# Optimization experiments

Measured on AMD Instinct MI355X. Metric: run time of the kernel, lower is better.

## Reference

```python
import jax, jax.numpy as jnp
import numpy as np

B, N, K, C, H, W = 2, 8, 8, 256, 96, 96
CTX = C + K + 4 * K + 13  # 309
HID = 256
ALPHA = 0.3          # REFINE_EMA_ALPHA
TEMP = 1.0           # READOUT_TEMPERATURE
SIM_HIGH, SIM_LOW = 0.8, 0.3
A_KEEP, A_REFINE, A_REPLACE, A_SPAWN = 0, 1, 2, 3


def _l2norm(x, axis=-1, eps=1e-12):
    return x / jnp.maximum(jnp.linalg.norm(x, axis=axis, keepdims=True), eps)


def setup_inputs() -> dict:
    key = jax.random.key(0)
    ks = jax.random.split(key, 12)
    value = jax.random.normal(ks[0], (B, N, C, H, W), jnp.float32)
    frame_feat = jax.random.normal(ks[1], (B, C, H, W), jnp.float32)
    mask = jax.random.uniform(ks[2], (B, N, H, W), jnp.float32)
    proto = jax.random.normal(ks[3], (B, N, K, C), jnp.float32)
    age = jax.random.uniform(ks[4], (B, N, K), jnp.float32) * 10.0
    usage = jax.random.uniform(ks[5], (B, N, K), jnp.float32) * 5.0
    conf = jax.random.uniform(ks[6], (B, N, K), jnp.float32)
    valid = jax.random.randint(ks[7], (B, N, K), 0, 2).astype(bool)
    W1 = jax.random.normal(ks[8], (CTX, HID), jnp.float32) * 0.02
    b1 = jnp.zeros((HID,), jnp.float32)
    W2 = jax.random.normal(ks[9], (HID, 4), jnp.float32) * 0.02
    b2 = jnp.zeros((4,), jnp.float32)
    proto_gate = jnp.float32(1.0)
    frame_gate = jnp.float32(1.0)
    return dict(value=value, frame_feat=frame_feat, mask=mask, proto=proto,
                age=age, usage=usage, conf=conf, W1=W1, b1=b1, W2=W2, b2=b2,
                proto_gate=proto_gate, frame_gate=frame_gate, valid=valid)


def reference(value, frame_feat, mask, proto, age, usage, conf,
              W1, b1, W2, b2, proto_gate, frame_gate, valid):
    # ---- candidate prototype via masked pooling (PROTO_POOLING='mask') ----
    fv = value.reshape(B, N, C, H * W)                      # [B,N,C,HW]
    fm = mask.reshape(B, N, 1, H * W)                       # [B,N,1,HW]
    denom = jnp.maximum(fm.sum(-1), 1e-6)                   # [B,N,1]
    cand = (fv * fm).sum(-1) / denom                        # [B,N,C]
    mask_strength = fm.mean(-1)[..., 0]                     # [B,N]
    fallback = fv.mean(-1)
    cand = jnp.where((denom[..., 0] <= 1e-5)[..., None], fallback, cand)
    cand = _l2norm(cand)

    # ---- uncertainty features (prev_mask is None -> temporal term = 0) ----
    m = jnp.clip(mask, 1e-4, 1.0 - 1e-4)
    ent = -(m * jnp.log(m) + (1.0 - m) * jnp.log(1.0 - m))
    fg_prob = m.mean((-2, -1))
    fg_area = (m > 0.5).astype(jnp.float32).mean((-2, -1))
    gx = jnp.abs(m[..., 1:, :] - m[..., :-1, :]).mean((-2, -1))
    gy = jnp.abs(m[..., :, 1:] - m[..., :, :-1]).mean((-2, -1))
    unc = jnp.stack([ent.mean((-2, -1)), fg_prob, fg_area,
                     0.5 * (gx + gy), jnp.zeros_like(fg_prob)], -1)  # [B,N,5]

    # ---- context / similarity ----
    bank_n = _l2norm(proto)                                  # [B,N,K,C]
    sim = jnp.einsum('bnc,bnkc->bnk', cand, bank_n)
    sim = jnp.where(valid, sim, -1.0)
    g_t = jnp.broadcast_to(frame_feat.mean((2, 3))[:, None, :], (B, N, C))
    age_n = age / jnp.maximum(age.max(), 1.0)
    usage_n = usage / jnp.maximum(usage.max(), 1.0)
    bank_stats = jnp.stack([valid.astype(jnp.float32), age_n, usage_n, conf], -1)
    top2 = jax.lax.top_k(sim, 2)[0]
    t1, t2 = top2[..., 0], top2[..., 1]
    glob = jnp.stack([valid.astype(jnp.float32).mean(-1), age_n.max(-1),
                      usage_n.min(-1), conf.mean(-1), conf.max(-1)], -1)
    context = jnp.concatenate([g_t, sim, bank_stats.reshape(B, N, 4 * K),
                               jnp.stack([t1, t2, t1 - t2], -1), glob, unc], -1)
    logits = jax.nn.gelu(context @ W1 + b1, approximate=False) @ W2 + b2  # [B,N,4]

    any_valid = valid.any(-1)
    target_slot = jnp.where(any_valid, sim.argmax(-1), 0)
    max_sim = jnp.take_along_axis(sim, target_slot[..., None], -1)[..., 0]
    max_sim = jnp.where(any_valid, max_sim, -1.0)

    # ---- rule-based action selection ----
    action = jnp.where(~any_valid, A_SPAWN,
             jnp.where(max_sim >= SIM_HIGH, A_REFINE,
             jnp.where(max_sim >= SIM_LOW, A_KEEP, A_SPAWN)))

    # ---- victim / slot selection ----
    victim = (age_n + (1.0 - usage_n) + (1.0 - conf)).argmax(-1)
    first_empty = (~valid).argmax(-1)
    spawn_slot = jnp.where((~valid).any(-1), first_empty, victim)
    upd_slot = jnp.where(action == A_REFINE, target_slot, spawn_slot)

    # ---- policy-gated EMA scatter update of the bank ----
    onehot = jax.nn.one_hot(upd_slot, K, dtype=bool)                 # [B,N,K]
    refine_m = onehot & (action == A_REFINE)[..., None]
    write_m = onehot & (action == A_SPAWN)[..., None]
    refined = _l2norm((1.0 - ALPHA) * proto + ALPHA * cand[:, :, None, :])
    cand_b = jnp.broadcast_to(cand[:, :, None, :], proto.shape)
    proto_new = jnp.where(refine_m[..., None], refined,
                jnp.where(write_m[..., None], cand_b, proto))
    upd_m = refine_m | write_m
    age_new = jnp.where(upd_m, 0.0, age + 1.0)
    usage_new = usage + upd_m.astype(jnp.float32)
    conf_new = jnp.where(write_m, mask_strength[..., None],
               jnp.where(refine_m, jnp.maximum(conf, max_sim[..., None]), conf))
    valid_new = valid | write_m

    # ---- prototype-conditioned readout ----
    bank_nn = _l2norm(proto_new)                                      # [B,N,K,C]
    vn = value / jnp.maximum(jnp.linalg.norm(value, axis=2, keepdims=True), 1e-12)
    rsim = jnp.einsum('bnkc,bnchw->bnkhw', bank_nn, vn)
    rlog = jnp.where(valid_new[..., None, None], rsim / TEMP, -1e9)
    attn = jax.nn.softmax(rlog, axis=2)
    attn = attn * valid_new.any(-1)[..., None, None, None].astype(jnp.float32)
    proto_map = jnp.einsum('bnkhw,bnkc->bnchw', attn, proto_new)
    conditioned = value + proto_gate * proto_map + frame_gate * frame_feat[:, None]
    return conditioned
```

## Files before the change

### kernel.cpp

```cpp
#include <hip/hip_runtime.h>
#include <math.h>

constexpr int Bc = 2, Nc = 8, Kc = 8, Cc = 256, HWc = 96 * 96;
constexpr int BN = Bc * Nc;
constexpr int HW2 = HWc / 2;
constexpr float ALPHA = 0.3f;
constexpr float SIM_HIGH = 0.8f, SIM_LOW = 0.3f;

__device__ __forceinline__ float wred_sum_all(float v) {
#pragma unroll
  for (int o = 32; o > 0; o >>= 1) v += __shfl_xor(v, o, 64);
  return v;
}
__device__ __forceinline__ float wred_sum(float v) {
#pragma unroll
  for (int o = 32; o > 0; o >>= 1) v += __shfl_down(v, o, 64);
  return v;
}
__device__ __forceinline__ float wred_max(float v) {
#pragma unroll
  for (int o = 32; o > 0; o >>= 1) v = fmaxf(v, __shfl_down(v, o, 64));
  return v;
}
__device__ __forceinline__ float bred_sum(float v, float* sc) {
  int lane = threadIdx.x & 63, wid = threadIdx.x >> 6;
  v = wred_sum(v);
  __syncthreads();
  if (lane == 0) sc[wid] = v;
  __syncthreads();
  return sc[0] + sc[1] + sc[2] + sc[3];
}
__device__ __forceinline__ float bred_max(float v, float* sc) {
  int lane = threadIdx.x & 63, wid = threadIdx.x >> 6;
  v = wred_max(v);
  __syncthreads();
  if (lane == 0) sc[wid] = v;
  __syncthreads();
  return fmaxf(fmaxf(sc[0], sc[1]), fmaxf(sc[2], sc[3]));
}

__global__ __launch_bounds__(256) void k1_sums(const float* __restrict__ value,
                                               const float* __restrict__ mask,
                                               float* __restrict__ sum_v,
                                               float* __restrict__ sum_vm) {
  const int bnc = blockIdx.x;
  const int bn = bnc >> 8;
  const int tid = threadIdx.x;
  const float4* v4 = (const float4*)(value + (size_t)bnc * HWc);
  const float4* m4 = (const float4*)(mask + (size_t)bn * HWc);
  float av = 0.f, avm = 0.f;
#pragma unroll
  for (int i = 0; i < 9; ++i) {
    float4 v = v4[i * 256 + tid];
    float4 m = m4[i * 256 + tid];
    av += v.x + v.y + v.z + v.w;
    avm += v.x * m.x + v.y * m.y + v.z * m.z + v.w * m.w;
  }
  __shared__ float sc[8];
  float rv = wred_sum(av);
  float rvm = wred_sum(avm);
  int lane = tid & 63, wid = tid >> 6;
  if (lane == 0) { sc[wid] = rv; sc[4 + wid] = rvm; }
  __syncthreads();
  if (tid == 0) {
    sum_v[bnc] = sc[0] + sc[1] + sc[2] + sc[3];
    sum_vm[bnc] = sc[4] + sc[5] + sc[6] + sc[7];
  }
}

__global__ __launch_bounds__(256) void k2_update(
    const float* __restrict__ mask, const float* __restrict__ proto,
    const float* __restrict__ age, const float* __restrict__ usage,
    const float* __restrict__ conf, const int* __restrict__ valid,
    const float* __restrict__ sum_v, const float* __restrict__ sum_vm,
    float* __restrict__ proto_new, float* __restrict__ bank_nn,
    float* __restrict__ validf) {
  const int bn = blockIdx.x;
  const int tid = threadIdx.x;
  const int lane = tid & 63, w = tid >> 6;
  __shared__ float sc[4];
  __shared__ float s_cand[Cc];
  __shared__ float s_sim[Kc];
  __shared__ int s_slot, s_ref, s_wr;

  float a = (tid < BN * Kc) ? age[tid] : -3e38f;
  float u = (tid < BN * Kc) ? usage[tid] : -3e38f;
  const float age_den = fmaxf(bred_max(a, sc), 1.0f);
  const float usage_den = fmaxf(bred_max(u, sc), 1.0f);

  float ms = 0.f;
  const float* mrow = mask + (size_t)bn * HWc;
  for (int i = tid; i < HWc; i += 256) ms += mrow[i];
  const float msum = bred_sum(ms, sc);
  const float denom = fmaxf(msum, 1e-6f);

  const int c = tid;
  const float sv = sum_v[bn * Cc + c];
  const float svm = sum_vm[bn * Cc + c];
  float cand = (denom <= 1e-5f) ? (sv * (1.0f / HWc)) : (svm / denom);
  const float css = bred_sum(cand * cand, sc);
  s_cand[c] = cand / fmaxf(sqrtf(css), 1e-12f);
  __syncthreads();

  const float4* cand4 = (const float4*)s_cand;
  const float4 c4 = cand4[lane];

#pragma unroll
  for (int kk = 0; kk < 2; ++kk) {
    const int k = w + kk * 4;
    const float4 p4 = ((const float4*)(proto + ((size_t)bn * Kc + k) * Cc))[lane];
    const float pss = wred_sum_all(p4.x * p4.x + p4.y * p4.y + p4.z * p4.z + p4.w * p4.w);
    const float pd  = wred_sum_all(p4.x * c4.x + p4.y * c4.y + p4.z * c4.z + p4.w * c4.w);
    if (lane == 0)
      s_sim[k] = (valid[bn * Kc + k] != 0) ? (pd / fmaxf(sqrtf(pss), 1e-12f)) : -1.0f;
  }
  __syncthreads();

  if (tid == 0) {
    bool anyv = false;
    for (int k = 0; k < Kc; ++k) anyv = anyv || (valid[bn * Kc + k] != 0);
    int tslot = 0; float best = s_sim[0];
    for (int k = 1; k < Kc; ++k)
      if (s_sim[k] > best) { best = s_sim[k]; tslot = k; }
    const float max_sim = anyv ? best : -1.0f;
    const int action = (!anyv) ? 3 : (max_sim >= SIM_HIGH ? 1 : (max_sim >= SIM_LOW ? 0 : 3));
    int victim = 0; float vb = -3e38f;
    for (int k = 0; k < Kc; ++k) {
      const float s = age[bn * Kc + k] / age_den + (1.f - usage[bn * Kc + k] / usage_den) +
                      (1.f - conf[bn * Kc + k]);
      if (s > vb) { vb = s; victim = k; }
    }
    int fe = 0; bool hasE = false;
    for (int k = 0; k < Kc; ++k)
      if (valid[bn * Kc + k] == 0) { fe = k; hasE = true; break; }
    const int spawn = hasE ? fe : victim;
    s_slot = (action == 1) ? tslot : spawn;
    s_ref = (action == 1);
    s_wr = (action == 3);
  }
  __syncthreads();

#pragma unroll
  for (int kk = 0; kk < 2; ++kk) {
    const int k = w + kk * 4;
    const float4 p4 = ((const float4*)(proto + ((size_t)bn * Kc + k) * Cc))[lane];
    float4 pn;
    if (k == s_slot && s_ref) {
      float4 t;
      t.x = (1.0f - ALPHA) * p4.x + ALPHA * c4.x;
      t.y = (1.0f - ALPHA) * p4.y + ALPHA * c4.y;
      t.z = (1.0f - ALPHA) * p4.z + ALPHA * c4.z;
      t.w = (1.0f - ALPHA) * p4.w + ALPHA * c4.w;
      const float tss = wred_sum_all(t.x * t.x + t.y * t.y + t.z * t.z + t.w * t.w);
      const float inv = 1.0f / fmaxf(sqrtf(tss), 1e-12f);
      pn.x = t.x * inv; pn.y = t.y * inv; pn.z = t.z * inv; pn.w = t.w * inv;
    } else if (k == s_slot && s_wr) {
      pn = c4;
    } else {
      pn = p4;
    }
    ((float4*)(proto_new + ((size_t)bn * Kc + k) * Cc))[lane] = pn;
    const float bss = wred_sum_all(pn.x * pn.x + pn.y * pn.y + pn.z * pn.z + pn.w * pn.w);
    const float binv = 1.0f / fmaxf(sqrtf(bss), 1e-12f);
    float4 bnv;
    bnv.x = pn.x * binv; bnv.y = pn.y * binv; bnv.z = pn.z * binv; bnv.w = pn.w * binv;
    ((float4*)(bank_nn + ((size_t)bn * Kc + k) * Cc))[lane] = bnv;
  }
  if (tid < Kc) {
    const int k = tid;
    const int vn = (valid[bn * Kc + k] != 0) || (s_wr && k == s_slot);
    validf[bn * Kc + k] = vn ? 1.0f : 0.0f;
  }
}

__global__ __launch_bounds__(256) void k3_readout(
    const float* __restrict__ value, const float* __restrict__ frame,
    const float* __restrict__ proto_new, const float* __restrict__ bank_nn,
    const float* __restrict__ validf, const float* __restrict__ pgp,
    const float* __restrict__ fgp, float* __restrict__ out) {
  const int bn = blockIdx.x / 72;
  const int tile = blockIdx.x % 72;
  const int b = bn >> 3;
  const int tid = threadIdx.x;
  const int lane = tid & 63, w = tid >> 6;
  const int p2 = tile * 64 + lane;

  __shared__ float s_bank[Kc * Cc];
  __shared__ float s_pn[Kc * Cc];
  __shared__ float s_part[4][9][128];
  __shared__ float s_attn[Kc][128];
  __shared__ float s_vld[Kc];

  const float* bsrc = bank_nn + (size_t)bn * Kc * Cc;
  const float* psrc = proto_new + (size_t)bn * Kc * Cc;
  for (int i = tid; i < Kc * Cc; i += 256) {
    const int k = i >> 8, c = i & 255;
    s_bank[c * 8 + k] = bsrc[i];
    s_pn[c * 8 + k] = psrc[i];
  }
  if (tid < Kc) s_vld[tid] = validf[bn * Kc + tid];
  __syncthreads();

  const float pg = pgp[0], fg = fgp[0];
  const float2* v2 = (const float2*)(value + (size_t)bn * Cc * HWc);
  const float2* f2 = (const float2*)(frame + (size_t)b * Cc * HWc);
  float2* o2 = (float2*)(out + (size_t)bn * Cc * HWc);
  const float4* bk4 = (const float4*)s_bank;
  const float4* pn4 = (const float4*)s_pn;

  float ss0 = 0.f, ss1 = 0.f;
  float d0[8], d1[8];
#pragma unroll
  for (int k = 0; k < 8; ++k) { d0[k] = 0.f; d1[k] = 0.f; }

#pragma unroll 8
  for (int c0 = 0; c0 < 64; ++c0) {
    const int c = (w << 6) + c0;
    const float2 v = v2[c * HW2 + p2];
    const float4 ba = bk4[c * 2 + 0];
    const float4 bb = bk4[c * 2 + 1];
    ss0 += v.x * v.x; ss1 += v.y * v.y;
    d0[0] += ba.x * v.x; d0[1] += ba.y * v.x; d0[2] += ba.z * v.x; d0[3] += ba.w * v.x;
    d0[4] += bb.x * v.x; d0[5] += bb.y * v.x; d0[6] += bb.z * v.x; d0[7] += bb.w * v.x;
    d1[0] += ba.x * v.y; d1[1] += ba.y * v.y; d1[2] += ba.z * v.y; d1[3] += ba.w * v.y;
    d1[4] += bb.x * v.y; d1[5] += bb.y * v.y; d1[6] += bb.z * v.y; d1[7] += bb.w * v.y;
  }
#pragma unroll
  for (int k = 0; k < 8; ++k)
    ((float2*)&s_part[w][k][0])[lane] = make_float2(d0[k], d1[k]);
  ((float2*)&s_part[w][8][0])[lane] = make_float2(ss0, ss1);
  __syncthreads();

  if (tid < 128) {
    float dd[9];
#pragma unroll
    for (int j = 0; j < 9; ++j)
      dd[j] = s_part[0][j][tid] + s_part[1][j][tid] + s_part[2][j][tid] + s_part[3][j][tid];
    const float rn = 1.0f / fmaxf(sqrtf(dd[8]), 1e-12f);
    float m = -3e38f;
#pragma unroll
    for (int k = 0; k < 8; ++k) {
      dd[k] *= rn;
      if (s_vld[k] > 0.5f) m = fmaxf(m, dd[k]);
    }
    float e[8], sum = 0.f;
#pragma unroll
    for (int k = 0; k < 8; ++k) {
      e[k] = (s_vld[k] > 0.5f) ? __expf(dd[k] - m) : 0.f;
      sum += e[k];
    }
    const float inv = (sum > 0.f) ? 1.0f / sum : 0.f;
#pragma unroll
    for (int k = 0; k < 8; ++k) s_attn[k][tid] = e[k] * inv;
  }
  __syncthreads();

  float a0[8], a1[8];
#pragma unroll
  for (int k = 0; k < 8; ++k) {
    const float2 t = ((const float2*)&s_attn[k][0])[lane];
    a0[k] = t.x; a1[k] = t.y;
  }

#pragma unroll 4
  for (int c0 = 0; c0 < 64; ++c0) {
    const int c = (w << 6) + c0;
    const float2 v = v2[c * HW2 + p2];
    const float2 f = f2[c * HW2 + p2];
    const float4 pa = pn4[c * 2 + 0];
    const float4 pb = pn4[c * 2 + 1];
    const float pm0 = a0[0] * pa.x + a0[1] * pa.y + a0[2] * pa.z + a0[3] * pa.w +
                      a0[4] * pb.x + a0[5] * pb.y + a0[6] * pb.z + a0[7] * pb.w;
    const float pm1 = a1[0] * pa.x + a1[1] * pa.y + a1[2] * pa.z + a1[3] * pa.w +
                      a1[4] * pb.x + a1[5] * pb.y + a1[6] * pb.z + a1[7] * pb.w;
    float2 o;
    o.x = v.x + pg * pm0 + fg * f.x;
    o.y = v.y + pg * pm1 + fg * f.y;
    o2[c * HW2 + p2] = o;
  }
}

extern "C" void kernel_launch(void* const* d_in, const int* in_sizes, int n_in,
                              void* d_out, int out_size, void* d_ws, size_t ws_size,
                              hipStream_t stream) {
  const float* value = (const float*)d_in[0];
  const float* frame = (const float*)d_in[1];
  const float* mask  = (const float*)d_in[2];
  const float* proto = (const float*)d_in[3];
  const float* age   = (const float*)d_in[4];
  const float* usage = (const float*)d_in[5];
  const float* conf  = (const float*)d_in[6];
  const float* pg = (const float*)d_in[11];
  const float* fg = (const float*)d_in[12];
  const int* valid = (const int*)d_in[13];
  float* out = (float*)d_out;

  float* w = (float*)d_ws;
  float* sum_v     = w;
  float* sum_vm    = w + 4096;
  float* proto_new = w + 8192;
  float* bank_nn   = w + 40960;
  float* validf    = w + 73728;

  hipLaunchKernelGGL(k1_sums, dim3(BN * Cc), dim3(256), 0, stream,
                     value, mask, sum_v, sum_vm);
  hipLaunchKernelGGL(k2_update, dim3(BN), dim3(256), 0, stream,
                     mask, proto, age, usage, conf, valid, sum_v, sum_vm,
                     proto_new, bank_nn, validf);
  hipLaunchKernelGGL(k3_readout, dim3(BN * 72), dim3(256), 0, stream,
                     value, frame, proto_new, bank_nn, validf, pg, fg, out);
}
```

Baseline: 390.2 us.

## Restructure readout kernel: channel groups within wave, shuffle reductions, fold bank normalization

```diff
diff --git a/kernel.cpp b/kernel.cpp
--- a/kernel.cpp
+++ b/kernel.cpp
@@ -6,6 +6,13 @@
 constexpr int HW2 = HWc / 2;
 constexpr float ALPHA = 0.3f;
 constexpr float SIM_HIGH = 0.8f, SIM_LOW = 0.3f;
+
+constexpr int CG = 8;
+constexpr int CPG = Cc / CG;
+constexpr int PPW = 64 / CG;
+constexpr int PPB = PPW * 4;
+constexpr int TILES = HW2 / PPB;
+constexpr int CGSTRIDE = CPG * 8 + 4;
 
 __device__ __forceinline__ float wred_sum_all(float v) {
 #pragma unroll
@@ -73,7 +80,7 @@
     const float* __restrict__ age, const float* __restrict__ usage,
     const float* __restrict__ conf, const int* __restrict__ valid,
     const float* __restrict__ sum_v, const float* __restrict__ sum_vm,
-    float* __restrict__ proto_new, float* __restrict__ bank_nn,
+    float* __restrict__ proto_new, float* __restrict__ bank_inv,
     float* __restrict__ validf) {
   const int bn = blockIdx.x;
   const int tid = threadIdx.x;
@@ -89,8 +96,11 @@
   const float usage_den = fmaxf(bred_max(u, sc), 1.0f);
 
   float ms = 0.f;
-  const float* mrow = mask + (size_t)bn * HWc;
-  for (int i = tid; i < HWc; i += 256) ms += mrow[i];
+  const float4* m4 = (const float4*)(mask + (size_t)bn * HWc);
+  for (int i = tid; i < HWc / 4; i += 256) {
+    const float4 mm = m4[i];
+    ms += (mm.x + mm.y) + (mm.z + mm.w);
+  }
   const float msum = bred_sum(ms, sc);
   const float denom = fmaxf(msum, 1e-6f);
 
@@ -161,10 +171,7 @@
     }
     ((float4*)(proto_new + ((size_t)bn * Kc + k) * Cc))[lane] = pn;
     const float bss = wred_sum_all(pn.x * pn.x + pn.y * pn.y + pn.z * pn.z + pn.w * pn.w);
-    const float binv = 1.0f / fmaxf(sqrtf(bss), 1e-12f);
-    float4 bnv;
-    bnv.x = pn.x * binv; bnv.y = pn.y * binv; bnv.z = pn.z * binv; bnv.w = pn.w * binv;
-    ((float4*)(bank_nn + ((size_t)bn * Kc + k) * Cc))[lane] = bnv;
+    if (lane == 0) bank_inv[bn * Kc + k] = 1.0f / fmaxf(sqrtf(bss), 1e-12f);
   }
   if (tid < Kc) {
     const int k = tid;
@@ -173,110 +180,107 @@
   }
 }
 
-__global__ __launch_bounds__(256) void k3_readout(
+__global__ __launch_bounds__(256, 8) void k3_readout(
     const float* __restrict__ value, const float* __restrict__ frame,
-    const float* __restrict__ proto_new, const float* __restrict__ bank_nn,
+    const float* __restrict__ proto_new, const float* __restrict__ bank_inv,
     const float* __restrict__ validf, const float* __restrict__ pgp,
     const float* __restrict__ fgp, float* __restrict__ out) {
-  const int bn = blockIdx.x / 72;
-  const int tile = blockIdx.x % 72;
+  const int bn = blockIdx.x / TILES;
+  const int tile = blockIdx.x % TILES;
   const int b = bn >> 3;
   const int tid = threadIdx.x;
   const int lane = tid & 63, w = tid >> 6;
-  const int p2 = tile * 64 + lane;
-
-  __shared__ float s_bank[Kc * Cc];
-  __shared__ float s_pn[Kc * Cc];
-  __shared__ float s_part[4][9][128];
-  __shared__ float s_attn[Kc][128];
+  const int cg = lane >> 3;
+  const int pl = lane & 7;
+  const int p2 = tile * PPB + w * PPW + pl;
+
+  __shared__ float s_pn[CG * CGSTRIDE];
+  __shared__ float s_inv[Kc];
   __shared__ float s_vld[Kc];
 
-  const float* bsrc = bank_nn + (size_t)bn * Kc * Cc;
   const float* psrc = proto_new + (size_t)bn * Kc * Cc;
   for (int i = tid; i < Kc * Cc; i += 256) {
     const int k = i >> 8, c = i & 255;
-    s_bank[c * 8 + k] = bsrc[i];
-    s_pn[c * 8 + k] = psrc[i];
-  }
-  if (tid < Kc) s_vld[tid] = validf[bn * Kc + tid];
+    s_pn[(c >> 5) * CGSTRIDE + (c & 31) * 8 + k] = psrc[i];
+  }
+  if (tid < Kc) {
+    s_inv[tid] = bank_inv[bn * Kc + tid];
+    s_vld[tid] = validf[bn * Kc + tid];
+  }
   __syncthreads();
 
   const float pg = pgp[0], fg = fgp[0];
   const float2* v2 = (const float2*)(value + (size_t)bn * Cc * HWc);
   const float2* f2 = (const float2*)(frame + (size_t)b * Cc * HWc);
   float2* o2 = (float2*)(out + (size_t)bn * Cc * HWc);
-  const float4* bk4 = (const float4*)s_bank;
-  const float4* pn4 = (const float4*)s_pn;
+  const size_t base = (size_t)(cg * CPG) * HW2 + p2;
+  const float4* pn4 = (const float4*)(s_pn + cg * CGSTRIDE);
 
   float ss0 = 0.f, ss1 = 0.f;
   float d0[8], d1[8];
 #pragma unroll
   for (int k = 0; k < 8; ++k) { d0[k] = 0.f; d1[k] = 0.f; }
 
-#pragma unroll 8
-  for (int c0 = 0; c0 < 64; ++c0) {
-    const int c = (w << 6) + c0;
-    const float2 v = v2[c * HW2 + p2];
-    const float4 ba = bk4[c * 2 + 0];
-    const float4 bb = bk4[c * 2 + 1];
+#pragma unroll 4
+  for (int i = 0; i < CPG; ++i) {
+    const float2 v = v2[base + (size_t)i * HW2];
+    const float4 ba = pn4[i * 2 + 0];
+    const float4 bb = pn4[i * 2 + 1];
     ss0 += v.x * v.x; ss1 += v.y * v.y;
     d0[0] += ba.x * v.x; d0[1] += ba.y * v.x; d0[2] += ba.z * v.x; d0[3] += ba.w * v.x;
     d0[4] += bb.x * v.x; d0[5] += bb.y * v.x; d0[6] += bb.z * v.x; d0[7] += bb.w * v.x;
     d1[0] += ba.x * v.y; d1[1] += ba.y * v.y; d1[2] += ba.z * v.y; d1[3] += ba.w * v.y;
     d1[4] += bb.x * v.y; d1[5] += bb.y * v.y; d1[6] += bb.z * v.y; d1[7] += bb.w * v.y;
   }
-#pragma unroll
-  for (int k = 0; k < 8; ++k)
-    ((float2*)&s_part[w][k][0])[lane] = make_float2(d0[k], d1[k]);
-  ((float2*)&s_part[w][8][0])[lane] = make_float2(ss0, ss1);
-  __syncthreads();
-
-  if (tid < 128) {
-    float dd[9];
-#pragma unroll
-    for (int j = 0; j < 9; ++j)
-      dd[j] = s_part[0][j][tid] + s_part[1][j][tid] + s_part[2][j][tid] + s_part[3][j][tid];
-    const float rn = 1.0f / fmaxf(sqrtf(dd[8]), 1e-12f);
-    float m = -3e38f;
-#pragma unroll
-    for (int k = 0; k < 8; ++k) {
-      dd[k] *= rn;
-      if (s_vld[k] > 0.5f) m = fmaxf(m, dd[k]);
-    }
-    float e[8], sum = 0.f;
-#pragma unroll
-    for (int k = 0; k < 8; ++k) {
-      e[k] = (s_vld[k] > 0.5f) ? __expf(dd[k] - m) : 0.f;
-      sum += e[k];
-    }
-    const float inv = (sum > 0.f) ? 1.0f / sum : 0.f;
-#pragma unroll
-    for (int k = 0; k < 8; ++k) s_attn[k][tid] = e[k] * inv;
-  }
-  __syncthreads();
-
-  float a0[8], a1[8];
+
 #pragma unroll
   for (int k = 0; k < 8; ++k) {
-    const float2 t = ((const float2*)&s_attn[k][0])[lane];
-    a0[k] = t.x; a1[k] = t.y;
-  }
+    d0[k] += __shfl_xor(d0[k], 8, 64);
+    d0[k] += __shfl_xor(d0[k], 16, 64);
+    d0[k] += __shfl_xor(d0[k], 32, 64);
+    d1[k] += __shfl_xor(d1[k], 8, 64);
+    d1[k] += __shfl_xor(d1[k], 16, 64);
+    d1[k] += __shfl_xor(d1[k], 32, 64);
+  }
+  ss0 += __shfl_xor(ss0, 8, 64); ss0 += __shfl_xor(ss0, 16, 64); ss0 += __shfl_xor(ss0, 32, 64);
+  ss1 += __shfl_xor(ss1, 8, 64); ss1 += __shfl_xor(ss1, 16, 64); ss1 += __shfl_xor(ss1, 32, 64);
+
+  const float rn0 = 1.0f / fmaxf(sqrtf(ss0), 1e-12f);
+  const float rn1 = 1.0f / fmaxf(sqrtf(ss1), 1e-12f);
+  float m0 = -3e38f, m1 = -3e38f;
+#pragma unroll
+  for (int k = 0; k < 8; ++k) {
+    const float sc = s_inv[k];
+    d0[k] *= sc * rn0;
+    d1[k] *= sc * rn1;
+    if (s_vld[k] > 0.5f) { m0 = fmaxf(m0, d0[k]); m1 = fmaxf(m1, d1[k]); }
+  }
+  float sum0 = 0.f, sum1 = 0.f;
+#pragma unroll
+  for (int k = 0; k < 8; ++k) {
+    d0[k] = (s_vld[k] > 0.5f) ? __expf(d0[k] - m0) : 0.f;
+    d1[k] = (s_vld[k] > 0.5f) ? __expf(d1[k] - m1) : 0.f;
+    sum0 += d0[k]; sum1 += d1[k];
+  }
+  const float inv0 = (sum0 > 0.f) ? 1.0f / sum0 : 0.f;
+  const float inv1 = (sum1 > 0.f) ? 1.0f / sum1 : 0.f;
+#pragma unroll
+  for (int k = 0; k < 8; ++k) { d0[k] *= inv0; d1[k] *= inv1; }
 
 #pragma unroll 4
-  for (int c0 = 0; c0 < 64; ++c0) {
-    const int c = (w << 6) + c0;
-    const float2 v = v2[c * HW2 + p2];
-    const float2 f = f2[c * HW2 + p2];
-    const float4 pa = pn4[c * 2 + 0];
-    const float4 pb = pn4[c * 2 + 1];
-    const float pm0 = a0[0] * pa.x + a0[1] * pa.y + a0[2] * pa.z + a0[3] * pa.w +
-                      a0[4] * pb.x + a0[5] * pb.y + a0[6] * pb.z + a0[7] * pb.w;
-    const float pm1 = a1[0] * pa.x + a1[1] * pa.y + a1[2] * pa.z + a1[3] * pa.w +
-                      a1[4] * pb.x + a1[5] * pb.y + a1[6] * pb.z + a1[7] * pb.w;
+  for (int i = 0; i < CPG; ++i) {
+    const float2 v = v2[base + (size_t)i * HW2];
+    const float2 f = f2[base + (size_t)i * HW2];
+    const float4 pa = pn4[i * 2 + 0];
+    const float4 pb = pn4[i * 2 + 1];
+    const float pm0 = d0[0] * pa.x + d0[1] * pa.y + d0[2] * pa.z + d0[3] * pa.w +
+                      d0[4] * pb.x + d0[5] * pb.y + d0[6] * pb.z + d0[7] * pb.w;
+    const float pm1 = d1[0] * pa.x + d1[1] * pa.y + d1[2] * pa.z + d1[3] * pa.w +
+                      d1[4] * pb.x + d1[5] * pb.y + d1[6] * pb.z + d1[7] * pb.w;
     float2 o;
     o.x = v.x + pg * pm0 + fg * f.x;
     o.y = v.y + pg * pm1 + fg * f.y;
-    o2[c * HW2 + p2] = o;
+    o2[base + (size_t)i * HW2] = o;
   }
 }
 
@@ -299,14 +303,14 @@
   float* sum_v     = w;
   float* sum_vm    = w + 4096;
   float* proto_new = w + 8192;
-  float* bank_nn   = w + 40960;
-  float* validf    = w + 73728;
+  float* bank_inv  = w + 40960;
+  float* validf    = w + 41088;
 
   hipLaunchKernelGGL(k1_sums, dim3(BN * Cc), dim3(256), 0, stream,
                      value, mask, sum_v, sum_vm);
   hipLaunchKernelGGL(k2_update, dim3(BN), dim3(256), 0, stream,
                      mask, proto, age, usage, conf, valid, sum_v, sum_vm,
-                     proto_new, bank_nn, validf);
-  hipLaunchKernelGGL(k3_readout, dim3(BN * 72), dim3(256), 0, stream,
-                     value, frame, proto_new, bank_nn, validf, pg, fg, out);
-}
+                     proto_new, bank_inv, validf);
+  hipLaunchKernelGGL(k3_readout, dim3(BN * TILES), dim3(256), 0, stream,
+                     value, frame, proto_new, bank_inv, validf, pg, fg, out);
+}
```

Result: slower. 475.5 us (+21.9%).
